# Kernel optimization log

Hardware: AMD Instinct MI355X
Metric: run time of the kernel (lower is better)

## Reference

```python
import jax, jax.numpy as jnp
import numpy as np

B, S, D_IN, D, H = 2, 2048, 512, 1024, 16
HD = D // H


def _linear_params(key, d_in, d_out):
    kw, kb = jax.random.split(key)
    bound = 1.0 / np.sqrt(d_in)
    W = jax.random.uniform(kw, (d_in, d_out), jnp.float32, -bound, bound)
    b = jax.random.uniform(kb, (d_out,), jnp.float32, -bound, bound)
    return W, b


def setup_inputs() -> dict:
    key = jax.random.key(0)
    keys = jax.random.split(key, 8)
    x = jax.random.normal(keys[0], (B, S, D_IN), jnp.float32)
    We, be = _linear_params(keys[1], D_IN, D)
    Wq, bq = _linear_params(keys[2], D, D)
    Wk, bk = _linear_params(keys[3], D, D)
    Wv, bv = _linear_params(keys[4], D, D)
    W0, b0 = _linear_params(keys[5], D, D)
    W1, b1 = _linear_params(keys[6], D, D)
    W2, b2 = _linear_params(keys[7], D, D)
    return {"x": x, "We": We, "be": be, "Wq": Wq, "bq": bq, "Wk": Wk, "bk": bk,
            "Wv": Wv, "bv": bv, "W0": W0, "b0": b0, "W1": W1, "b1": b1, "W2": W2, "b2": b2}


def reference(x, We, be, Wq, bq, Wk, bk, Wv, bv, W0, b0, W1, b1, W2, b2):
    # embedding
    e = x @ We + be                                   # [B,S,D]
    q = (e @ Wq + bq).reshape(B, S, H, HD)            # [B,S,H,hd]
    k = (e @ Wk + bk).reshape(B, S, H, HD)
    v = (e @ Wv + bv).reshape(B, S, H, HD)
    scale = 1.0 / jnp.sqrt(jnp.float32(HD))
    scores = jnp.einsum('bqhd,bkhd->bhqk', q, k) * scale
    attn = jax.nn.softmax(scores, axis=-1)            # [B,H,S,S]
    ctx = jnp.einsum('bhqk,bkhd->bqhd', attn, v).reshape(B, S, D)
    mha = e + (ctx @ W0 + b0)                         # residual
    ffn = jax.nn.relu(mha @ W1 + b1) @ W2 + b2
    return mha + ffn
```

## Files before the change

### kernel.cpp

```cpp
#include <hip/hip_runtime.h>

typedef unsigned short u16;
typedef __bf16 bf16x8 __attribute__((ext_vector_type(8)));
typedef float f32x4 __attribute__((ext_vector_type(4)));

__device__ __forceinline__ float bf2f(u16 u) {
  return __builtin_bit_cast(float, (unsigned)u << 16);
}
__device__ __forceinline__ u16 f2bf(float f) {
  unsigned u = __builtin_bit_cast(unsigned, f);
  u += 0x7FFFu + ((u >> 16) & 1u);
  return (u16)(u >> 16);
}
__device__ __forceinline__ unsigned pk2(float a, float b) {
  return (unsigned)f2bf(a) | ((unsigned)f2bf(b) << 16);
}
__device__ __forceinline__ unsigned pk2t(float a, float b) {
  return __builtin_amdgcn_perm(__builtin_bit_cast(unsigned, b),
                               __builtin_bit_cast(unsigned, a), 0x07060302u);
}
__device__ __forceinline__ f32x4 mfma16(bf16x8 a, bf16x8 b, f32x4 c) {
  return __builtin_amdgcn_mfma_f32_16x16x32_bf16(a, b, c, 0, 0, 0);
}
__device__ __forceinline__ void async_cp16(const u16* g, u16* l) {
  __builtin_amdgcn_global_load_lds((const __attribute__((address_space(1))) void*)g,
                                   (__attribute__((address_space(3))) void*)l, 16, 0, 0);
}
#define S_BARRIER() asm volatile("s_barrier" ::: "memory")

__global__ __launch_bounds__(256) void cast_f32_bf16(const float* __restrict__ in,
                                                     u16* __restrict__ out, int n) {
  int idx = (blockIdx.x * 256 + threadIdx.x) * 4;
  if (idx < n) {
    float4 f = *(const float4*)&in[idx];
    ushort4 o;
    o.x = f2bf(f.x); o.y = f2bf(f.y); o.z = f2bf(f.z); o.w = f2bf(f.w);
    *(ushort4*)&out[idx] = o;
  }
}

__global__ __launch_bounds__(256) void biascat(const float* __restrict__ bq,
                                               const float* __restrict__ bk,
                                               const float* __restrict__ bv,
                                               float* __restrict__ o) {
  int i = blockIdx.x * 256 + threadIdx.x;
  if (i < 3072)
    o[i] = i < 1024 ? bq[i] : (i < 2048 ? bk[i - 1024] : bv[i - 2048]);
}

#define TSP 72
__global__ __launch_bounds__(256) void transpose_weights(
    const float* __restrict__ We, const float* __restrict__ Wq,
    const float* __restrict__ Wk, const float* __restrict__ Wv,
    const float* __restrict__ W0, const float* __restrict__ W1,
    const float* __restrict__ W2, u16* Wet, u16* qkvWt, u16* W0t, u16* W1t,
    u16* W2t) {
  const int z = blockIdx.z;
  const float* in;
  u16* out;
  int Kc = 128;
  if (z == 0) { if (blockIdx.y >= 8) return; in = We; out = Wet; Kc = 64; }
  else if (z == 1) { in = Wq; out = qkvWt; }
  else if (z == 2) { in = Wk; out = qkvWt + 1048576; }
  else if (z == 3) { in = Wv; out = qkvWt + 2097152; }
  else if (z == 4) { in = W0; out = W0t; }
  else if (z == 5) { in = W1; out = W1t; }
  else { in = W2; out = W2t; }
  __shared__ alignas(16) u16 T[64][TSP];
  const int tid = threadIdx.x;
  const int r0 = blockIdx.y * 64, c0 = blockIdx.x * 64;
#pragma unroll
  for (int it = 0; it < 4; ++it) {
    int vi = it * 256 + tid;
    int i = vi >> 4, j4 = (vi & 15) * 4;
    float4 f = *(const float4*)&in[(size_t)(r0 + i) * 1024 + c0 + j4];
    T[i][j4 + 0] = f2bf(f.x);
    T[i][j4 + 1] = f2bf(f.y);
    T[i][j4 + 2] = f2bf(f.z);
    T[i][j4 + 3] = f2bf(f.w);
  }
  __syncthreads();
#pragma unroll
  for (int it = 0; it < 2; ++it) {
    int vi = it * 256 + tid;
    int n_loc = vi >> 3, kcl = vi & 7;
    bf16x8 v;
#pragma unroll
    for (int u = 0; u < 8; ++u) ((u16*)&v)[u] = T[kcl * 8 + u][n_loc];
    int nt16 = (c0 + n_loc) >> 4;
    int kc = (r0 >> 3) + kcl;
    *(bf16x8*)&out[(((size_t)nt16 * Kc + kc) * 16 + (n_loc & 15)) * 8] = v;
  }
}

__global__ __launch_bounds__(256, 3) void gemm_mfma(
    const u16* __restrict__ A, const u16* __restrict__ Bp,
    const float* __restrict__ bias, const u16* __restrict__ res,
    void* __restrict__ Cout, int M, int N, int K, int relu, int f32out) {
  __shared__ alignas(16) u16 As[2][64 * 64];
  const int tid = threadIdx.x;
  const int wave = tid >> 6, lane = tid & 63;
  const int quad = lane >> 4, l16 = lane & 15;
  const int ib = blockIdx.x;
  const int by = (ib & 7) * 8 + ((ib >> 3) & 7);
  const int bx = ib >> 6;
  const int m0 = by * 64, n0 = bx * 128;
  const int wm = (wave & 1) * 32, wn16 = (wave >> 1) * 4;
  const int Kc = K >> 3;

  f32x4 acc[2][4];
#pragma unroll
  for (int i = 0; i < 2; ++i)
#pragma unroll
    for (int j = 0; j < 4; ++j) acc[i][j] = (f32x4){0.f, 0.f, 0.f, 0.f};

  const int srow = lane >> 3;
  const int schunk = (lane & 7) ^ (srow & 7);
  const u16* Ag = A + (size_t)(m0 + wave * 16 + srow) * K + schunk * 8;
  u16* AsW0 = &As[0][wave * 16 * 64];
  u16* AsW1 = &As[1][wave * 16 * 64];
  const u16* Bpw = Bp + ((size_t)(n0 / 16 + wn16) * Kc) * 128 + l16 * 8;

  bf16x8 a00, a01, a02, a03, a10, a11, a12, a13;
  bf16x8 b00, b01, b02, b03, b10, b11, b12, b13;

#define ISSUE_A(ab, k)                                    \
  {                                                       \
    async_cp16(Ag + (k), (ab));                           \
    async_cp16(Ag + (k) + (size_t)8 * K, (ab) + 512);     \
  }
#define BADDR(kk, nt, k0c) \
  (*(const bf16x8*)&Bpw[((size_t)(nt)*Kc + (k0c) + (kk)*4 + quad) * 128])
#define LOAD_B(p, k0c)                                                  \
  {                                                                     \
    p##00 = BADDR(0, 0, k0c); p##01 = BADDR(0, 1, k0c);                 \
    p##02 = BADDR(0, 2, k0c); p##03 = BADDR(0, 3, k0c);                 \
    p##10 = BADDR(1, 0, k0c); p##11 = BADDR(1, 1, k0c);                 \
    p##12 = BADDR(1, 2, k0c); p##13 = BADDR(1, 3, k0c);                 \
  }
#define COMPUTE(cb, p)                                                  \
  {                                                                     \
    bf16x8 af0, af1;                                                    \
    af0 = *(const bf16x8*)&As[cb][(wm + l16) * 64 + (quad ^ swz) * 8];  \
    af1 = *(const bf16x8*)&As[cb][(wm + 16 + l16) * 64 + (quad ^ swz) * 8]; \
    acc[0][0] = mfma16(af0, p##00, acc[0][0]);                          \
    acc[0][1] = mfma16(af0, p##01, acc[0][1]);                          \
    acc[0][2] = mfma16(af0, p##02, acc[0][2]);                          \
    acc[0][3] = mfma16(af0, p##03, acc[0][3]);                          \
    acc[1][0] = mfma16(af1, p##00, acc[1][0]);                          \
    acc[1][1] = mfma16(af1, p##01, acc[1][1]);                          \
    acc[1][2] = mfma16(af1, p##02, acc[1][2]);                          \
    acc[1][3] = mfma16(af1, p##03, acc[1][3]);                          \
    af0 = *(const bf16x8*)&As[cb][(wm + l16) * 64 + ((4 + quad) ^ swz) * 8]; \
    af1 = *(const bf16x8*)&As[cb][(wm + 16 + l16) * 64 + ((4 + quad) ^ swz) * 8]; \
    acc[0][0] = mfma16(af0, p##10, acc[0][0]);                          \
    acc[0][1] = mfma16(af0, p##11, acc[0][1]);                          \
    acc[0][2] = mfma16(af0, p##12, acc[0][2]);                          \
    acc[0][3] = mfma16(af0, p##13, acc[0][3]);                          \
    acc[1][0] = mfma16(af1, p##10, acc[1][0]);                          \
    acc[1][1] = mfma16(af1, p##11, acc[1][1]);                          \
    acc[1][2] = mfma16(af1, p##12, acc[1][2]);                          \
    acc[1][3] = mfma16(af1, p##13, acc[1][3]);                          \
  }

  ISSUE_A(AsW0, 0);
  LOAD_B(a, 0);
  const int T = K >> 6;
  const int swz = (l16 & 7);
  for (int t = 0; t < T; t += 2) {
    S_BARRIER();
    {
      const int kn = (t + 1) << 6;
      ISSUE_A(AsW1, kn);
      LOAD_B(b, kn >> 3);
    }
    asm volatile("s_waitcnt vmcnt(10)" ::: "memory");
    S_BARRIER();
    COMPUTE(0, a);
    S_BARRIER();
    {
      const int kn = (t + 2 < T) ? ((t + 2) << 6) : 0;
      ISSUE_A(AsW0, kn);
      LOAD_B(a, kn >> 3);
    }
    asm volatile("s_waitcnt vmcnt(10)" ::: "memory");
    S_BARRIER();
    COMPUTE(1, b);
  }
  asm volatile("s_waitcnt vmcnt(0)" ::: "memory");

#pragma unroll
  for (int nt = 0; nt < 4; ++nt) {
    int col = n0 + wn16 * 16 + nt * 16 + l16;
    float bv = bias[col];
#pragma unroll
    for (int mt = 0; mt < 2; ++mt) {
#pragma unroll
      for (int r = 0; r < 4; ++r) {
        int row = m0 + wm + mt * 16 + quad * 4 + r;
        float v = acc[mt][nt][r] + bv;
        if (res) v += bf2f(res[(size_t)row * N + col]);
        if (relu) v = fmaxf(v, 0.f);
        if (f32out)
          ((float*)Cout)[(size_t)row * N + col] = v;
        else
          ((u16*)Cout)[(size_t)row * N + col] = f2bf(v);
      }
    }
  }
}

__global__ __launch_bounds__(256, 2) void attn_kernel(
    const u16* __restrict__ QKV, const u16* __restrict__ Vt,
    u16* __restrict__ O) {
  __shared__ alignas(16) u16 Ks[2][64 * 64];
  __shared__ alignas(16) u16 Vs[2][64 * 64];
  __shared__ alignas(16) u16 Ps[4][32 * 72];
  const int tid = threadIdx.x;
  const int wave = tid >> 6, lane = tid & 63;
  const int quad = lane >> 4, l16 = lane & 15;
  const int ib = blockIdx.x;
  const int bh = ib & 31, b = bh >> 4, h = bh & 15;
  const int q0 = (ib >> 5) * 128 + wave * 32;

  bf16x8 qf[2][2];
#pragma unroll
  for (int qt = 0; qt < 2; ++qt) {
    const size_t qoff = (size_t)(b * 2048 + q0 + qt * 16 + l16) * 3072 + h * 64;
#pragma unroll
    for (int kk = 0; kk < 2; ++kk) {
      bf16x8 raw = *(const bf16x8*)&QKV[qoff + kk * 32 + quad * 8];
#pragma unroll
      for (int u = 0; u < 8; ++u)
        ((u16*)&raw)[u] = f2bf(0.125f * bf2f(((u16*)&raw)[u]));
      qf[qt][kk] = raw;
    }
  }
  bf16x8 ones;
#pragma unroll
  for (int u = 0; u < 8; ++u) ((u16*)&ones)[u] = 0x3F80;

  f32x4 o[4][2];
  f32x4 l_acc[2] = {(f32x4){0.f, 0.f, 0.f, 0.f}, (f32x4){0.f, 0.f, 0.f, 0.f}};
#pragma unroll
  for (int mt = 0; mt < 4; ++mt)
#pragma unroll
    for (int qt = 0; qt < 2; ++qt) o[mt][qt] = (f32x4){0.f, 0.f, 0.f, 0.f};

  const int srow = lane >> 3;
  const int schunk = (lane & 7) ^ (srow & 7);
  const u16* Kg = QKV + (size_t)(b * 2048 + wave * 16 + srow) * 3072 + 1024 +
                  h * 64 + schunk * 8;
  const u16* Vg = Vt + (size_t)((b * 16 + h) * 64 + wave * 16 + srow) * 2048 +
                  schunk * 8;
  u16* KsW0 = &Ks[0][(wave * 16) * 64];
  u16* VsW0 = &Vs[0][(wave * 16) * 64];
  u16* KsW1 = &Ks[1][(wave * 16) * 64];
  u16* VsW1 = &Vs[1][(wave * 16) * 64];

#define ATTN_ISSUE(kb, vb, kt)                                \
  {                                                           \
    async_cp16(Kg + (size_t)(kt) * 3072, (kb));               \
    async_cp16(Kg + (size_t)((kt) + 8) * 3072, (kb) + 512);   \
    async_cp16(Vg + (kt), (vb));                              \
    async_cp16(Vg + (kt) + (size_t)8 * 2048, (vb) + 512);     \
  }

  ATTN_ISSUE(KsW0, VsW0, 0);
  const int swz = (l16 & 7);
  u16* PsW = &Ps[wave][0];
  for (int t = 0; t < 32; ++t) {
    const int cb = t & 1;
    S_BARRIER();
    const int ktn = (t + 1 < 32) ? ((t + 1) * 64) : 0;
    if (cb == 0) ATTN_ISSUE(KsW1, VsW1, ktn) else ATTN_ISSUE(KsW0, VsW0, ktn);
    asm volatile("s_waitcnt vmcnt(4)" ::: "memory");
    S_BARRIER();

    f32x4 st[4][2];
#pragma unroll
    for (int km = 0; km < 4; ++km)
#pragma unroll
      for (int qt = 0; qt < 2; ++qt) st[km][qt] = (f32x4){0.f, 0.f, 0.f, 0.f};
#pragma unroll
    for (int kk = 0; kk < 2; ++kk)
#pragma unroll
      for (int km = 0; km < 4; ++km) {
        bf16x8 kf = *(const bf16x8*)&Ks[cb][(km * 16 + l16) * 64 +
                                           ((kk * 4 + quad) ^ swz) * 8];
        st[km][0] = mfma16(kf, qf[0][kk], st[km][0]);
        st[km][1] = mfma16(kf, qf[1][kk], st[km][1]);
      }

#pragma unroll
    for (int qt = 0; qt < 2; ++qt)
#pragma unroll
      for (int km = 0; km < 4; ++km) {
        float e0 = __expf(st[km][qt][0]), e1 = __expf(st[km][qt][1]);
        float e2 = __expf(st[km][qt][2]), e3 = __expf(st[km][qt][3]);
        uint2 pk;
        pk.x = pk2t(e0, e1);
        pk.y = pk2t(e2, e3);
        *(uint2*)&PsW[(qt * 16 + l16) * 72 + km * 16 + quad * 4] = pk;
      }
    asm volatile("s_waitcnt lgkmcnt(0)" ::: "memory");

#pragma unroll
    for (int kk2 = 0; kk2 < 2; ++kk2) {
      bf16x8 pf0 = *(const bf16x8*)&PsW[l16 * 72 + kk2 * 32 + quad * 8];
      bf16x8 pf1 = *(const bf16x8*)&PsW[(16 + l16) * 72 + kk2 * 32 + quad * 8];
      l_acc[0] = mfma16(ones, pf0, l_acc[0]);
      l_acc[1] = mfma16(ones, pf1, l_acc[1]);
#pragma unroll
      for (int mt = 0; mt < 4; ++mt) {
        bf16x8 vf = *(const bf16x8*)&Vs[cb][(mt * 16 + l16) * 64 +
                                           ((kk2 * 4 + quad) ^ swz) * 8];
        o[mt][0] = mfma16(vf, pf0, o[mt][0]);
        o[mt][1] = mfma16(vf, pf1, o[mt][1]);
      }
    }
  }
  asm volatile("s_waitcnt vmcnt(0)" ::: "memory");

#pragma unroll
  for (int qt = 0; qt < 2; ++qt) {
    float inv = 1.f / l_acc[qt][0];
    size_t base = (size_t)(b * 2048 + q0 + qt * 16 + l16) * 1024 + h * 64;
#pragma unroll
    for (int mt = 0; mt < 4; ++mt) {
      uint2 pk;
      pk.x = pk2(o[mt][qt][0] * inv, o[mt][qt][1] * inv);
      pk.y = pk2(o[mt][qt][2] * inv, o[mt][qt][3] * inv);
      *(uint2*)&O[base + mt * 16 + quad * 4] = pk;
    }
  }
}

__global__ __launch_bounds__(256) void transpose_v(const u16* __restrict__ QKV,
                                                   u16* __restrict__ vt) {
  const int bh = blockIdx.y;
  const int b = bh >> 4, h = bh & 15;
  const int s0 = blockIdx.x * 64;
  const u16* in = QKV + (size_t)b * 2048 * 3072 + 2048 + h * 64;
  u16* out = vt + (size_t)bh * 131072;
  __shared__ alignas(16) u16 T[64][TSP];
  const int tid = threadIdx.x;
#pragma unroll
  for (int it = 0; it < 2; ++it) {
    int vi = it * 256 + tid;
    int i = vi >> 3, j8 = (vi & 7) * 8;
    *(bf16x8*)&T[i][j8] = *(const bf16x8*)&in[(size_t)(s0 + i) * 3072 + j8];
  }
  __syncthreads();
#pragma unroll
  for (int it = 0; it < 2; ++it) {
    int vi = it * 256 + tid;
    int i = vi >> 3, j8 = (vi & 7) * 8;
    bf16x8 vv;
#pragma unroll
    for (int u = 0; u < 8; ++u) ((u16*)&vv)[u] = T[j8 + u][i];
    *(bf16x8*)&out[(size_t)i * 2048 + s0 + j8] = vv;
  }
}

extern "C" void kernel_launch(void* const* d_in, const int* in_sizes, int n_in,
                              void* d_out, int out_size, void* d_ws,
                              size_t ws_size, hipStream_t stream) {
  const float* x = (const float*)d_in[0];
  const float* We = (const float*)d_in[1];
  const float* be = (const float*)d_in[2];
  const float* Wq = (const float*)d_in[3];
  const float* bq = (const float*)d_in[4];
  const float* Wk = (const float*)d_in[5];
  const float* bk = (const float*)d_in[6];
  const float* Wv = (const float*)d_in[7];
  const float* bv = (const float*)d_in[8];
  const float* W0 = (const float*)d_in[9];
  const float* b0 = (const float*)d_in[10];
  const float* W1 = (const float*)d_in[11];
  const float* b1 = (const float*)d_in[12];
  const float* W2 = (const float*)d_in[13];
  const float* b2 = (const float*)d_in[14];

  u16* ws = (u16*)d_ws;
  u16* xb = ws;
  u16* Wet = xb + 2097152;
  u16* qkvWt = Wet + 524288;
  u16* ctx = ws;
  u16* W0t = qkvWt + 3145728;
  u16* W1t = W0t + 1048576;
  u16* W2t = W1t + 1048576;
  float* biasqkv = (float*)(W2t + 1048576);
  u16* e = W2t + 1048576 + 6144;
  u16* qkv = e + 4194304;
  u16* vtb = qkv + 12582912;
  u16* mha = qkv;
  u16* h1 = e;

  cast_f32_bf16<<<2048, 256, 0, stream>>>(x, xb, 4096 * 512);
  transpose_weights<<<dim3(16, 16, 7), 256, 0, stream>>>(
      We, Wq, Wk, Wv, W0, W1, W2, Wet, qkvWt, W0t, W1t, W2t);
  biascat<<<12, 256, 0, stream>>>(bq, bk, bv, biasqkv);

  gemm_mfma<<<512, 256, 0, stream>>>(xb, Wet, be, nullptr, e, 4096, 1024, 512,
                                     0, 0);
  gemm_mfma<<<1536, 256, 0, stream>>>(e, qkvWt, biasqkv, nullptr, qkv, 4096,
                                      3072, 1024, 0, 0);
  transpose_v<<<dim3(32, 32), 256, 0, stream>>>(qkv, vtb);
  attn_kernel<<<512, 256, 0, stream>>>(qkv, vtb, ctx);
  gemm_mfma<<<512, 256, 0, stream>>>(ctx, W0t, b0, e, mha, 4096, 1024, 1024, 0,
                                     0);
  gemm_mfma<<<512, 256, 0, stream>>>(mha, W1t, b1, nullptr, h1, 4096, 1024,
                                     1024, 1, 0);
  gemm_mfma<<<512, 256, 0, stream>>>(h1, W2t, b2, mha, d_out, 4096, 1024, 1024,
                                     0, 1);
}
```

Baseline: 272.2 us.

## Double per-wave query tile in attention and triple-buffer K/V loads

```diff
diff --git a/kernel.cpp b/kernel.cpp
--- a/kernel.cpp
+++ b/kernel.cpp
@@ -210,22 +210,22 @@
   }
 }
 
-__global__ __launch_bounds__(256, 2) void attn_kernel(
+__global__ __launch_bounds__(256, 1) void attn_kernel(
     const u16* __restrict__ QKV, const u16* __restrict__ Vt,
     u16* __restrict__ O) {
-  __shared__ alignas(16) u16 Ks[2][64 * 64];
-  __shared__ alignas(16) u16 Vs[2][64 * 64];
-  __shared__ alignas(16) u16 Ps[4][32 * 72];
+  __shared__ alignas(16) u16 Ks[3][64 * 64];
+  __shared__ alignas(16) u16 Vs[3][64 * 64];
+  __shared__ alignas(16) u16 Ps[4][64 * 72];
   const int tid = threadIdx.x;
   const int wave = tid >> 6, lane = tid & 63;
   const int quad = lane >> 4, l16 = lane & 15;
   const int ib = blockIdx.x;
   const int bh = ib & 31, b = bh >> 4, h = bh & 15;
-  const int q0 = (ib >> 5) * 128 + wave * 32;
-
-  bf16x8 qf[2][2];
-#pragma unroll
-  for (int qt = 0; qt < 2; ++qt) {
+  const int q0 = (ib >> 5) * 256 + wave * 64;
+
+  bf16x8 qf[4][2];
+#pragma unroll
+  for (int qt = 0; qt < 4; ++qt) {
     const size_t qoff = (size_t)(b * 2048 + q0 + qt * 16 + l16) * 3072 + h * 64;
 #pragma unroll
     for (int kk = 0; kk < 2; ++kk) {
@@ -240,12 +240,14 @@
 #pragma unroll
   for (int u = 0; u < 8; ++u) ((u16*)&ones)[u] = 0x3F80;
 
-  f32x4 o[4][2];
-  f32x4 l_acc[2] = {(f32x4){0.f, 0.f, 0.f, 0.f}, (f32x4){0.f, 0.f, 0.f, 0.f}};
+  f32x4 o[4][4];
+  f32x4 l_acc[4];
 #pragma unroll
   for (int mt = 0; mt < 4; ++mt)
 #pragma unroll
-    for (int qt = 0; qt < 2; ++qt) o[mt][qt] = (f32x4){0.f, 0.f, 0.f, 0.f};
+    for (int qt = 0; qt < 4; ++qt) o[mt][qt] = (f32x4){0.f, 0.f, 0.f, 0.f};
+#pragma unroll
+  for (int qt = 0; qt < 4; ++qt) l_acc[qt] = (f32x4){0.f, 0.f, 0.f, 0.f};
 
   const int srow = lane >> 3;
   const int schunk = (lane & 7) ^ (srow & 7);
@@ -253,47 +255,48 @@
                   h * 64 + schunk * 8;
   const u16* Vg = Vt + (size_t)((b * 16 + h) * 64 + wave * 16 + srow) * 2048 +
                   schunk * 8;
-  u16* KsW0 = &Ks[0][(wave * 16) * 64];
-  u16* VsW0 = &Vs[0][(wave * 16) * 64];
-  u16* KsW1 = &Ks[1][(wave * 16) * 64];
-  u16* VsW1 = &Vs[1][(wave * 16) * 64];
-
-#define ATTN_ISSUE(kb, vb, kt)                                \
-  {                                                           \
-    async_cp16(Kg + (size_t)(kt) * 3072, (kb));               \
-    async_cp16(Kg + (size_t)((kt) + 8) * 3072, (kb) + 512);   \
-    async_cp16(Vg + (kt), (vb));                              \
-    async_cp16(Vg + (kt) + (size_t)8 * 2048, (vb) + 512);     \
-  }
-
-  ATTN_ISSUE(KsW0, VsW0, 0);
+  const int woff = wave * 16 * 64;
+
+#define ATTN_ISSUE(bufi, kt)                                        \
+  {                                                                 \
+    u16* kb = &Ks[bufi][woff];                                      \
+    u16* vb = &Vs[bufi][woff];                                      \
+    async_cp16(Kg + (size_t)(kt) * 3072, kb);                       \
+    async_cp16(Kg + (size_t)((kt) + 8) * 3072, kb + 512);           \
+    async_cp16(Vg + (kt), vb);                                      \
+    async_cp16(Vg + (kt) + (size_t)8 * 2048, vb + 512);             \
+  }
+
+  ATTN_ISSUE(0, 0);
+  ATTN_ISSUE(1, 64);
   const int swz = (l16 & 7);
   u16* PsW = &Ps[wave][0];
+  int cb = 0, pb = 2;
   for (int t = 0; t < 32; ++t) {
-    const int cb = t & 1;
-    S_BARRIER();
-    const int ktn = (t + 1 < 32) ? ((t + 1) * 64) : 0;
-    if (cb == 0) ATTN_ISSUE(KsW1, VsW1, ktn) else ATTN_ISSUE(KsW0, VsW0, ktn);
-    asm volatile("s_waitcnt vmcnt(4)" ::: "memory");
-    S_BARRIER();
-
-    f32x4 st[4][2];
+    S_BARRIER();
+    const int ktn = (t + 2 < 32) ? ((t + 2) * 64) : 0;
+    ATTN_ISSUE(pb, ktn);
+    asm volatile("s_waitcnt vmcnt(8)" ::: "memory");
+    S_BARRIER();
+
+    f32x4 st[4][4];
 #pragma unroll
     for (int km = 0; km < 4; ++km)
 #pragma unroll
-      for (int qt = 0; qt < 2; ++qt) st[km][qt] = (f32x4){0.f, 0.f, 0.f, 0.f};
+      for (int qt = 0; qt < 4; ++qt) st[km][qt] = (f32x4){0.f, 0.f, 0.f, 0.f};
 #pragma unroll
     for (int kk = 0; kk < 2; ++kk)
 #pragma unroll
       for (int km = 0; km < 4; ++km) {
         bf16x8 kf = *(const bf16x8*)&Ks[cb][(km * 16 + l16) * 64 +
                                            ((kk * 4 + quad) ^ swz) * 8];
-        st[km][0] = mfma16(kf, qf[0][kk], st[km][0]);
-        st[km][1] = mfma16(kf, qf[1][kk], st[km][1]);
+#pragma unroll
+        for (int qt = 0; qt < 4; ++qt)
+          st[km][qt] = mfma16(kf, qf[qt][kk], st[km][qt]);
       }
 
 #pragma unroll
-    for (int qt = 0; qt < 2; ++qt)
+    for (int qt = 0; qt < 4; ++qt)
 #pragma unroll
       for (int km = 0; km < 4; ++km) {
         float e0 = __expf(st[km][qt][0]), e1 = __expf(st[km][qt][1]);
@@ -307,23 +310,29 @@
 
 #pragma unroll
     for (int kk2 = 0; kk2 < 2; ++kk2) {
-      bf16x8 pf0 = *(const bf16x8*)&PsW[l16 * 72 + kk2 * 32 + quad * 8];
-      bf16x8 pf1 = *(const bf16x8*)&PsW[(16 + l16) * 72 + kk2 * 32 + quad * 8];
-      l_acc[0] = mfma16(ones, pf0, l_acc[0]);
-      l_acc[1] = mfma16(ones, pf1, l_acc[1]);
+      bf16x8 pf[4];
+#pragma unroll
+      for (int qt = 0; qt < 4; ++qt)
+        pf[qt] = *(const bf16x8*)&PsW[(qt * 16 + l16) * 72 + kk2 * 32 + quad * 8];
+#pragma unroll
+      for (int qt = 0; qt < 4; ++qt)
+        l_acc[qt] = mfma16(ones, pf[qt], l_acc[qt]);
 #pragma unroll
       for (int mt = 0; mt < 4; ++mt) {
         bf16x8 vf = *(const bf16x8*)&Vs[cb][(mt * 16 + l16) * 64 +
                                            ((kk2 * 4 + quad) ^ swz) * 8];
-        o[mt][0] = mfma16(vf, pf0, o[mt][0]);
-        o[mt][1] = mfma16(vf, pf1, o[mt][1]);
+#pragma unroll
+        for (int qt = 0; qt < 4; ++qt)
+          o[mt][qt] = mfma16(vf, pf[qt], o[mt][qt]);
       }
     }
+    cb = (cb == 2) ? 0 : cb + 1;
+    pb = (pb == 2) ? 0 : pb + 1;
   }
   asm volatile("s_waitcnt vmcnt(0)" ::: "memory");
 
 #pragma unroll
-  for (int qt = 0; qt < 2; ++qt) {
+  for (int qt = 0; qt < 4; ++qt) {
     float inv = 1.f / l_acc[qt][0];
     size_t base = (size_t)(b * 2048 + q0 + qt * 16 + l16) * 1024 + h * 64;
 #pragma unroll
@@ -407,7 +416,7 @@
   gemm_mfma<<<1536, 256, 0, stream>>>(e, qkvWt, biasqkv, nullptr, qkv, 4096,
                                       3072, 1024, 0, 0);
   transpose_v<<<dim3(32, 32), 256, 0, stream>>>(qkv, vtb);
-  attn_kernel<<<512, 256, 0, stream>>>(qkv, vtb, ctx);
+  attn_kernel<<<256, 256, 0, stream>>>(qkv, vtb, ctx);
   gemm_mfma<<<512, 256, 0, stream>>>(ctx, W0t, b0, e, mha, 4096, 1024, 1024, 0,
                                      0);
   gemm_mfma<<<512, 256, 0, stream>>>(mha, W1t, b1, nullptr, h1, 4096, 1024,
```

New measurement: 302.0 us. +11.0%, slower.
